# Optimization experiments

Measured on AMD Instinct MI355X. Metric: run time of the kernel, lower is better.

The kernel has to match this reference:

```python
import jax, jax.numpy as jnp
import numpy as np

B, S, H = 8, 2048, 768
VOCAB, MODAL_V, SEG_V, NPI_V, MAX_POS = 32000, 16, 4, 10000, 2048
LN_EPS = 1e-12


def _sinusoidal_table(max_pos, hidden):
    pos = np.arange(max_pos, dtype=np.float32)[:, None]          # [P,1]
    idx = np.arange(hidden, dtype=np.float32)[None, :]           # [1,H]
    angle = pos / np.power(10000.0, 2.0 * idx / hidden)          # even_code/odd_code share 2*idx/H exponent
    tab = np.where(np.arange(hidden)[None, :] % 2 == 0, np.sin(angle), np.cos(angle))
    return jnp.asarray(tab, dtype=jnp.float32)


def setup_inputs() -> dict:
    key = jax.random.key(0)
    ks = jax.random.split(key, 16)
    inp = {
        'word_ids': jax.random.randint(ks[0], (B, S), 0, VOCAB),
        'modalities_ids': jax.random.randint(ks[1], (B, S), 0, MODAL_V),
        'seg_ids': jax.random.randint(ks[2], (B, S), 0, SEG_V),
        'npi_ids': jax.random.randint(ks[3], (B, S), 0, NPI_V),
        'posi_ids': jnp.sort(jax.random.randint(ks[4], (B, S), 0, MAX_POS), axis=-1),
        'age_tau': jax.random.uniform(ks[5], (B, S), dtype=jnp.float32) * 100.0,
        'delays_tau': jax.random.uniform(ks[6], (B, S), dtype=jnp.float32) * 100.0,
        'word_table': jax.random.normal(ks[7], (VOCAB, H), dtype=jnp.float32) * 0.02,
        'modalities_table': jax.random.normal(ks[8], (MODAL_V, H), dtype=jnp.float32) * 0.02,
        'seg_table': jax.random.normal(ks[9], (SEG_V, H), dtype=jnp.float32) * 0.02,
        'npi_table': jax.random.normal(ks[10], (NPI_V, H), dtype=jnp.float32) * 0.02,
        'posi_table': _sinusoidal_table(MAX_POS, H),
        'age_w': jax.random.normal(ks[11], (1, H - 1), dtype=jnp.float32),
        'age_b': jax.random.normal(ks[12], (H - 1,), dtype=jnp.float32),
        'age_w0': jax.random.normal(ks[13], (1, 1), dtype=jnp.float32),
        'age_b0': jax.random.normal(ks[14], (1,), dtype=jnp.float32),
        'delay_w': jax.random.normal(ks[15], (1, H - 1), dtype=jnp.float32),
        'delay_b': jax.random.normal(jax.random.fold_in(key, 100), (H - 1,), dtype=jnp.float32),
        'delay_w0': jax.random.normal(jax.random.fold_in(key, 101), (1, 1), dtype=jnp.float32),
        'delay_b0': jax.random.normal(jax.random.fold_in(key, 102), (1,), dtype=jnp.float32),
        'ln_gamma': jnp.ones((H,), dtype=jnp.float32),
        'ln_beta': jnp.zeros((H,), dtype=jnp.float32),
    }
    return inp


def _time2vec(tau, w, b, w0, b0):
    # tau: [B,S] scalar times; w: [1,H-1]; w0: [1,1]. Vectorized SineActivation.
    t = tau[..., None]                      # [B,S,1]
    v1 = jnp.sin(t * w[0] + b)              # [B,S,H-1]
    v2 = t * w0[0] + b0                     # [B,S,1]
    return jnp.concatenate([v1, v2], axis=-1)


def _layer_norm(x, gamma, beta, eps):
    mu = jnp.mean(x, axis=-1, keepdims=True)
    var = jnp.mean(jnp.square(x - mu), axis=-1, keepdims=True)
    return (x - mu) * jax.lax.rsqrt(var + eps) * gamma + beta


def reference(word_ids, modalities_ids, seg_ids, npi_ids, posi_ids, age_tau, delays_tau,
              word_table, modalities_table, seg_table, npi_table, posi_table,
              age_w, age_b, age_w0, age_b0, delay_w, delay_b, delay_w0, delay_b0,
              ln_gamma, ln_beta):
    word_e = word_table[word_ids]
    seg_e = seg_table[seg_ids]
    modal_e = modalities_table[modalities_ids]
    npi_e = npi_table[npi_ids]
    posi_e = posi_table[posi_ids]
    age_e = _time2vec(age_tau, age_w, age_b, age_w0, age_b0)
    delay_e = _time2vec(delays_tau, delay_w, delay_b, delay_w0, delay_b0)
    # else-branch: sum of all seven embeddings
    emb = word_e + seg_e + posi_e + modal_e + delay_e + age_e + npi_e
    emb = _layer_norm(emb, ln_gamma, ln_beta, LN_EPS)
    return emb  # dropout is identity in eval mode
```

## Files before the change

### kernel.cpp

```cpp
#include <hip/hip_runtime.h>
#include <cmath>

static constexpr int B_ = 8;
static constexpr int S_ = 2048;
static constexpr int H_ = 768;
static constexpr int TOKENS = B_ * S_;
static constexpr float LN_EPS = 1e-12f;

typedef float nfloat4 __attribute__((ext_vector_type(4)));

__global__ __launch_bounds__(256, 4) void bert_emb_kernel(
    const int* __restrict__ word_ids,
    const int* __restrict__ modal_ids,
    const int* __restrict__ seg_ids,
    const int* __restrict__ npi_ids,
    const int* __restrict__ posi_ids,
    const float* __restrict__ age_tau,
    const float* __restrict__ delay_tau,
    const float* __restrict__ word_table,
    const float* __restrict__ modal_table,
    const float* __restrict__ seg_table,
    const float* __restrict__ npi_table,
    const float* __restrict__ posi_table,
    const float* __restrict__ age_w,
    const float* __restrict__ age_b,
    const float* __restrict__ age_w0,
    const float* __restrict__ age_b0,
    const float* __restrict__ delay_w,
    const float* __restrict__ delay_b,
    const float* __restrict__ delay_w0,
    const float* __restrict__ delay_b0,
    const float* __restrict__ ln_gamma,
    const float* __restrict__ ln_beta,
    float* __restrict__ out)
{
    const int wave = threadIdx.x >> 6;
    const int lane = threadIdx.x & 63;
    const int token = (blockIdx.x << 2) + wave;

    const int wid = word_ids[token];
    const int mid = modal_ids[token];
    const int sid = seg_ids[token];
    const int nid = npi_ids[token];
    const int pid = posi_ids[token];
    const float atau = age_tau[token];
    const float dtau = delay_tau[token];
    const float aw0 = age_w0[0], ab0 = age_b0[0];
    const float dw0 = delay_w0[0], db0 = delay_b0[0];

    const float4* wrow = reinterpret_cast<const float4*>(word_table  + (size_t)wid * H_);
    const float4* mrow = reinterpret_cast<const float4*>(modal_table + (size_t)mid * H_);
    const float4* srow = reinterpret_cast<const float4*>(seg_table   + (size_t)sid * H_);
    const float4* nrow = reinterpret_cast<const float4*>(npi_table   + (size_t)nid * H_);
    const float4* prow = reinterpret_cast<const float4*>(posi_table  + (size_t)pid * H_);
    const float4* awv = reinterpret_cast<const float4*>(age_w);
    const float4* abv = reinterpret_cast<const float4*>(age_b);
    const float4* dwv = reinterpret_cast<const float4*>(delay_w);
    const float4* dbv = reinterpret_cast<const float4*>(delay_b);

    float vals[12];
    float ssum = 0.0f, ssq = 0.0f;

#pragma unroll
    for (int c = 0; c < 3; ++c) {
        const int h4 = lane + (c << 6);
        const float4 we = wrow[h4];
        const float4 me = mrow[h4];
        const float4 se = srow[h4];
        const float4 ne = nrow[h4];
        const float4 pe = prow[h4];

        float4 aw, ab, dw, db;
        if (h4 < (H_ / 4 - 1)) {
            aw = awv[h4]; ab = abv[h4]; dw = dwv[h4]; db = dbv[h4];
        } else {
            aw = make_float4(age_w[764],   age_w[765],   age_w[766],   0.0f);
            ab = make_float4(age_b[764],   age_b[765],   age_b[766],   0.0f);
            dw = make_float4(delay_w[764], delay_w[765], delay_w[766], 0.0f);
            db = make_float4(delay_b[764], delay_b[765], delay_b[766], 0.0f);
        }

        float av0 = __sinf(atau * aw.x + ab.x);
        float av1 = __sinf(atau * aw.y + ab.y);
        float av2 = __sinf(atau * aw.z + ab.z);
        float av3 = __sinf(atau * aw.w + ab.w);
        float dv0 = __sinf(dtau * dw.x + db.x);
        float dv1 = __sinf(dtau * dw.y + db.y);
        float dv2 = __sinf(dtau * dw.z + db.z);
        float dv3 = __sinf(dtau * dw.w + db.w);
        if (h4 == (H_ / 4 - 1)) {
            av3 = atau * aw0 + ab0;
            dv3 = dtau * dw0 + db0;
        }

        const float e0 = we.x + me.x + se.x + ne.x + pe.x + av0 + dv0;
        const float e1 = we.y + me.y + se.y + ne.y + pe.y + av1 + dv1;
        const float e2 = we.z + me.z + se.z + ne.z + pe.z + av2 + dv2;
        const float e3 = we.w + me.w + se.w + ne.w + pe.w + av3 + dv3;

        vals[c * 4 + 0] = e0;
        vals[c * 4 + 1] = e1;
        vals[c * 4 + 2] = e2;
        vals[c * 4 + 3] = e3;
        ssum += e0 + e1 + e2 + e3;
        ssq  += e0 * e0 + e1 * e1 + e2 * e2 + e3 * e3;
    }

#pragma unroll
    for (int off = 32; off > 0; off >>= 1) {
        ssum += __shfl_down(ssum, off);
        ssq  += __shfl_down(ssq,  off);
    }
    ssum = __shfl(ssum, 0);
    ssq  = __shfl(ssq,  0);

    const float inv_h = 1.0f / (float)H_;
    const float mu = ssum * inv_h;
    const float var = ssq * inv_h - mu * mu;
    const float rstd = rsqrtf(var + LN_EPS);

    const float4* gv = reinterpret_cast<const float4*>(ln_gamma);
    const float4* bv = reinterpret_cast<const float4*>(ln_beta);
    nfloat4* orow = reinterpret_cast<nfloat4*>(out + (size_t)token * H_);

#pragma unroll
    for (int c = 0; c < 3; ++c) {
        const int h4 = lane + (c << 6);
        const float4 g  = gv[h4];
        const float4 bt = bv[h4];
        nfloat4 o;
        o.x = (vals[c * 4 + 0] - mu) * rstd * g.x + bt.x;
        o.y = (vals[c * 4 + 1] - mu) * rstd * g.y + bt.y;
        o.z = (vals[c * 4 + 2] - mu) * rstd * g.z + bt.z;
        o.w = (vals[c * 4 + 3] - mu) * rstd * g.w + bt.w;
        __builtin_nontemporal_store(o, &orow[h4]);
    }
}

extern "C" void kernel_launch(void* const* d_in, const int* in_sizes, int n_in,
                              void* d_out, int out_size, void* d_ws, size_t ws_size,
                              hipStream_t stream) {
    const int*   word_ids    = (const int*)  d_in[0];
    const int*   modal_ids   = (const int*)  d_in[1];
    const int*   seg_ids     = (const int*)  d_in[2];
    const int*   npi_ids     = (const int*)  d_in[3];
    const int*   posi_ids    = (const int*)  d_in[4];
    const float* age_tau     = (const float*)d_in[5];
    const float* delay_tau   = (const float*)d_in[6];
    const float* word_table  = (const float*)d_in[7];
    const float* modal_table = (const float*)d_in[8];
    const float* seg_table   = (const float*)d_in[9];
    const float* npi_table   = (const float*)d_in[10];
    const float* posi_table  = (const float*)d_in[11];
    const float* age_w       = (const float*)d_in[12];
    const float* age_b       = (const float*)d_in[13];
    const float* age_w0      = (const float*)d_in[14];
    const float* age_b0      = (const float*)d_in[15];
    const float* delay_w     = (const float*)d_in[16];
    const float* delay_b     = (const float*)d_in[17];
    const float* delay_w0    = (const float*)d_in[18];
    const float* delay_b0    = (const float*)d_in[19];
    const float* ln_gamma    = (const float*)d_in[20];
    const float* ln_beta     = (const float*)d_in[21];
    float* out = (float*)d_out;

    dim3 grid(TOKENS / 4);
    dim3 block(256);
    hipLaunchKernelGGL(bert_emb_kernel, grid, block, 0, stream,
                       word_ids, modal_ids, seg_ids, npi_ids, posi_ids,
                       age_tau, delay_tau,
                       word_table, modal_table, seg_table, npi_table, posi_table,
                       age_w, age_b, age_w0, age_b0,
                       delay_w, delay_b, delay_w0, delay_b0,
                       ln_gamma, ln_beta, out);
}
```

Before: 236.8 us.

## Map one token per 192-thread block with shared-memory reduction

Changes the work split from one wavefront per token (four tokens per block, three float4 chunks per lane) to one block of 192 threads per token, each thread handling a single float4. The layer-norm statistics are now reduced across three wavefronts through shared memory with a block barrier. The goal is to raise memory-level parallelism and occupancy by giving each thread less work and fewer registers, at the cost of four times as many blocks, a __syncthreads per token, and extra redundant loads of token ids.

```diff
diff --git a/kernel.cpp b/kernel.cpp
--- a/kernel.cpp
+++ b/kernel.cpp
@@ -9,7 +9,7 @@
 
 typedef float nfloat4 __attribute__((ext_vector_type(4)));
 
-__global__ __launch_bounds__(256, 4) void bert_emb_kernel(
+__global__ __launch_bounds__(192, 7) void bert_emb_kernel(
     const int* __restrict__ word_ids,
     const int* __restrict__ modal_ids,
     const int* __restrict__ seg_ids,
@@ -34,9 +34,12 @@
     const float* __restrict__ ln_beta,
     float* __restrict__ out)
 {
-    const int wave = threadIdx.x >> 6;
-    const int lane = threadIdx.x & 63;
-    const int token = (blockIdx.x << 2) + wave;
+    __shared__ float s_red[6];
+
+    const int token = blockIdx.x;
+    const int tid   = threadIdx.x;
+    const int wave  = tid >> 6;
+    const int lane  = tid & 63;
 
     const int wid = word_ids[token];
     const int mid = modal_ids[token];
@@ -45,96 +48,74 @@
     const int pid = posi_ids[token];
     const float atau = age_tau[token];
     const float dtau = delay_tau[token];
-    const float aw0 = age_w0[0], ab0 = age_b0[0];
-    const float dw0 = delay_w0[0], db0 = delay_b0[0];
 
-    const float4* wrow = reinterpret_cast<const float4*>(word_table  + (size_t)wid * H_);
-    const float4* mrow = reinterpret_cast<const float4*>(modal_table + (size_t)mid * H_);
-    const float4* srow = reinterpret_cast<const float4*>(seg_table   + (size_t)sid * H_);
-    const float4* nrow = reinterpret_cast<const float4*>(npi_table   + (size_t)nid * H_);
-    const float4* prow = reinterpret_cast<const float4*>(posi_table  + (size_t)pid * H_);
-    const float4* awv = reinterpret_cast<const float4*>(age_w);
-    const float4* abv = reinterpret_cast<const float4*>(age_b);
-    const float4* dwv = reinterpret_cast<const float4*>(delay_w);
-    const float4* dbv = reinterpret_cast<const float4*>(delay_b);
+    const float4 we = reinterpret_cast<const float4*>(word_table  + (size_t)wid * H_)[tid];
+    const float4 me = reinterpret_cast<const float4*>(modal_table + (size_t)mid * H_)[tid];
+    const float4 se = reinterpret_cast<const float4*>(seg_table   + (size_t)sid * H_)[tid];
+    const float4 ne = reinterpret_cast<const float4*>(npi_table   + (size_t)nid * H_)[tid];
+    const float4 pe = reinterpret_cast<const float4*>(posi_table  + (size_t)pid * H_)[tid];
 
-    float vals[12];
-    float ssum = 0.0f, ssq = 0.0f;
+    float4 aw, ab, dw, db;
+    if (tid < H_ / 4 - 1) {
+        aw = reinterpret_cast<const float4*>(age_w)[tid];
+        ab = reinterpret_cast<const float4*>(age_b)[tid];
+        dw = reinterpret_cast<const float4*>(delay_w)[tid];
+        db = reinterpret_cast<const float4*>(delay_b)[tid];
+    } else {
+        aw = make_float4(age_w[764],   age_w[765],   age_w[766],   0.0f);
+        ab = make_float4(age_b[764],   age_b[765],   age_b[766],   0.0f);
+        dw = make_float4(delay_w[764], delay_w[765], delay_w[766], 0.0f);
+        db = make_float4(delay_b[764], delay_b[765], delay_b[766], 0.0f);
+    }
 
-#pragma unroll
-    for (int c = 0; c < 3; ++c) {
-        const int h4 = lane + (c << 6);
-        const float4 we = wrow[h4];
-        const float4 me = mrow[h4];
-        const float4 se = srow[h4];
-        const float4 ne = nrow[h4];
-        const float4 pe = prow[h4];
+    float av0 = __sinf(atau * aw.x + ab.x);
+    float av1 = __sinf(atau * aw.y + ab.y);
+    float av2 = __sinf(atau * aw.z + ab.z);
+    float av3 = __sinf(atau * aw.w + ab.w);
+    float dv0 = __sinf(dtau * dw.x + db.x);
+    float dv1 = __sinf(dtau * dw.y + db.y);
+    float dv2 = __sinf(dtau * dw.z + db.z);
+    float dv3 = __sinf(dtau * dw.w + db.w);
+    if (tid == H_ / 4 - 1) {
+        av3 = atau * age_w0[0]   + age_b0[0];
+        dv3 = dtau * delay_w0[0] + delay_b0[0];
+    }
 
-        float4 aw, ab, dw, db;
-        if (h4 < (H_ / 4 - 1)) {
-            aw = awv[h4]; ab = abv[h4]; dw = dwv[h4]; db = dbv[h4];
-        } else {
-            aw = make_float4(age_w[764],   age_w[765],   age_w[766],   0.0f);
-            ab = make_float4(age_b[764],   age_b[765],   age_b[766],   0.0f);
-            dw = make_float4(delay_w[764], delay_w[765], delay_w[766], 0.0f);
-            db = make_float4(delay_b[764], delay_b[765], delay_b[766], 0.0f);
-        }
+    const float e0 = we.x + me.x + se.x + ne.x + pe.x + av0 + dv0;
+    const float e1 = we.y + me.y + se.y + ne.y + pe.y + av1 + dv1;
+    const float e2 = we.z + me.z + se.z + ne.z + pe.z + av2 + dv2;
+    const float e3 = we.w + me.w + se.w + ne.w + pe.w + av3 + dv3;
 
-        float av0 = __sinf(atau * aw.x + ab.x);
-        float av1 = __sinf(atau * aw.y + ab.y);
-        float av2 = __sinf(atau * aw.z + ab.z);
-        float av3 = __sinf(atau * aw.w + ab.w);
-        float dv0 = __sinf(dtau * dw.x + db.x);
-        float dv1 = __sinf(dtau * dw.y + db.y);
-        float dv2 = __sinf(dtau * dw.z + db.z);
-        float dv3 = __sinf(dtau * dw.w + db.w);
-        if (h4 == (H_ / 4 - 1)) {
-            av3 = atau * aw0 + ab0;
-            dv3 = dtau * dw0 + db0;
-        }
-
-        const float e0 = we.x + me.x + se.x + ne.x + pe.x + av0 + dv0;
-        const float e1 = we.y + me.y + se.y + ne.y + pe.y + av1 + dv1;
-        const float e2 = we.z + me.z + se.z + ne.z + pe.z + av2 + dv2;
-        const float e3 = we.w + me.w + se.w + ne.w + pe.w + av3 + dv3;
-
-        vals[c * 4 + 0] = e0;
-        vals[c * 4 + 1] = e1;
-        vals[c * 4 + 2] = e2;
-        vals[c * 4 + 3] = e3;
-        ssum += e0 + e1 + e2 + e3;
-        ssq  += e0 * e0 + e1 * e1 + e2 * e2 + e3 * e3;
-    }
+    float ssum = e0 + e1 + e2 + e3;
+    float ssq  = e0 * e0 + e1 * e1 + e2 * e2 + e3 * e3;
 
 #pragma unroll
     for (int off = 32; off > 0; off >>= 1) {
         ssum += __shfl_down(ssum, off);
         ssq  += __shfl_down(ssq,  off);
     }
-    ssum = __shfl(ssum, 0);
-    ssq  = __shfl(ssq,  0);
+    if (lane == 0) {
+        s_red[wave * 2 + 0] = ssum;
+        s_red[wave * 2 + 1] = ssq;
+    }
+    __syncthreads();
+    const float tsum = s_red[0] + s_red[2] + s_red[4];
+    const float tsq  = s_red[1] + s_red[3] + s_red[5];
 
     const float inv_h = 1.0f / (float)H_;
-    const float mu = ssum * inv_h;
-    const float var = ssq * inv_h - mu * mu;
+    const float mu = tsum * inv_h;
+    const float var = tsq * inv_h - mu * mu;
     const float rstd = rsqrtf(var + LN_EPS);
 
-    const float4* gv = reinterpret_cast<const float4*>(ln_gamma);
-    const float4* bv = reinterpret_cast<const float4*>(ln_beta);
+    const float4 g  = reinterpret_cast<const float4*>(ln_gamma)[tid];
+    const float4 bt = reinterpret_cast<const float4*>(ln_beta)[tid];
+    nfloat4 o;
+    o.x = (e0 - mu) * rstd * g.x + bt.x;
+    o.y = (e1 - mu) * rstd * g.y + bt.y;
+    o.z = (e2 - mu) * rstd * g.z + bt.z;
+    o.w = (e3 - mu) * rstd * g.w + bt.w;
     nfloat4* orow = reinterpret_cast<nfloat4*>(out + (size_t)token * H_);
-
-#pragma unroll
-    for (int c = 0; c < 3; ++c) {
-        const int h4 = lane + (c << 6);
-        const float4 g  = gv[h4];
-        const float4 bt = bv[h4];
-        nfloat4 o;
-        o.x = (vals[c * 4 + 0] - mu) * rstd * g.x + bt.x;
-        o.y = (vals[c * 4 + 1] - mu) * rstd * g.y + bt.y;
-        o.z = (vals[c * 4 + 2] - mu) * rstd * g.z + bt.z;
-        o.w = (vals[c * 4 + 3] - mu) * rstd * g.w + bt.w;
-        __builtin_nontemporal_store(o, &orow[h4]);
-    }
+    __builtin_nontemporal_store(o, &orow[tid]);
 }
 
 extern "C" void kernel_launch(void* const* d_in, const int* in_sizes, int n_in,
@@ -164,8 +145,8 @@
     const float* ln_beta     = (const float*)d_in[21];
     float* out = (float*)d_out;
 
-    dim3 grid(TOKENS / 4);
-    dim3 block(256);
+    dim3 grid(TOKENS);
+    dim3 block(192);
     hipLaunchKernelGGL(bert_emb_kernel, grid, block, 0, stream,
                        word_ids, modal_ids, seg_ids, npi_ids, posi_ids,
                        age_tau, delay_tau,
```

Result: slower. 255.5 us (+7.9%).
